# Optimization experiments

Measured on AMD Instinct MI355X. Metric: run time of the kernel, lower is better.

Reference implementation:

```python
import jax, jax.numpy as jnp
import numpy as np

EPS = 1e-09
TOP_K = 2


def setup_inputs() -> dict:
    key = jax.random.key(0)
    ks = jax.random.split(key, 6)
    B, L, F, E, D, SE = 64, 1024, 900, 8, 768, 64
    cycle_curve_data = jax.random.normal(ks[0], (B, L, F), dtype=jnp.float32)
    logits = jax.random.normal(ks[1], (B, E), dtype=jnp.float32)
    moe_masks = jax.random.randint(ks[2], (B, E), 0, 2, dtype=jnp.int32)
    selection_embeddings = jax.random.normal(ks[3], (B, E, SE), dtype=jnp.float32)
    W = jax.random.normal(ks[4], (E, F, D), dtype=jnp.float32) * 0.02
    b = jnp.zeros((E, D), dtype=jnp.float32)
    return {"cycle_curve_data": cycle_curve_data, "logits": logits,
            "moe_masks": moe_masks, "selection_embeddings": selection_embeddings,
            "W": W, "b": b}


def reference(cycle_curve_data, logits, moe_masks, selection_embeddings, W, b):
    B = cycle_curve_data.shape[0]
    E = logits.shape[1]
    mask = (moe_masks == 1).astype(logits.dtype)                 # [B, E]
    raw = jax.nn.softmax(logits, axis=1)                         # [B, E]
    p = raw * mask
    # selection embedding from inactive experts
    inactive = raw * (1.0 - mask)
    inactive = inactive / (jnp.sum(inactive, axis=1, keepdims=True) + EPS)
    selection_embedding = jnp.sum(selection_embeddings * inactive[:, :, None], axis=1)  # [B, SE]
    # top-k masking (indices treated as constants, same as torch scatter mask)
    if TOP_K > 0:
        _, idx = jax.lax.top_k(p, TOP_K)                         # [B, K]
        topk_mask = jnp.zeros_like(p).at[jnp.arange(B)[:, None], idx].set(1.0)
        p = p * topk_mask
    p = p / (jnp.sum(p, axis=1, keepdims=True) + EPS)            # [B, E]
    # dispatch/combine == weighted sum of per-expert Linear outputs
    # (weights are zero for unselected experts, matching MOEDispatcher)
    out = jnp.zeros(cycle_curve_data.shape[:2] + (W.shape[-1],), dtype=cycle_curve_data.dtype)
    for e in range(E):  # small fixed expert count
        expert_out = jnp.einsum('blf,fd->bld', cycle_curve_data, W[e]) + b[e]
        out = out + p[:, e, None, None] * expert_out
    final_out = out.astype(jnp.bfloat16)
    # guide loss (training mode)
    s = jnp.sum(raw * mask) / B
    guide_loss = (1.0 - s) * (1.0 - s)
    return final_out, guide_loss, selection_embedding
```

## Files before the change

kernel.cpp:

```cpp
#include <hip/hip_runtime.h>

#define B_  64
#define L_  1024
#define F_  900
#define E_  8
#define D_  768
#define SE_ 64
#define KP_ 928
#define FD_ (F_*D_)
#define OUT_MAIN (64*1024*768)
#define GL_OFF   OUT_MAIN
#define SE_OFF   (OUT_MAIN + 1)
#define EPSF 1e-9f


using f32x4  = __attribute__((ext_vector_type(4))) float;
using bf16   = __bf16;
using bf16x4 = __attribute__((ext_vector_type(4))) __bf16;
using bf16x8 = __attribute__((ext_vector_type(8))) __bf16;
using s16x8  = __attribute__((ext_vector_type(8))) short;

__device__ __forceinline__ f32x4 mfma_bf16(bf16x8 a, bf16x8 b, f32x4 c) {
  return __builtin_amdgcn_mfma_f32_16x16x32_bf16(
      __builtin_bit_cast(s16x8, a), __builtin_bit_cast(s16x8, b), c, 0, 0, 0);
}

__device__ __forceinline__ const unsigned* pick_masks(const void* cA, const void* cB,
                                                      const float** logits) {
  const unsigned* a = (const unsigned*)cA;
  bool aIsMask = true;
#pragma unroll
  for (int i = 0; i < 512; i += 37) aIsMask &= (a[i] <= 1u);
  if (aIsMask) { *logits = (const float*)cB; return a; }
  *logits = (const float*)cA; return (const unsigned*)cB;
}

struct Gate { int e1, e2; float p1, p2; };

__device__ __forceinline__ Gate gate_for(const float* __restrict__ logits,
                                         const unsigned* __restrict__ masks, int b) {
  float lg[E_]; unsigned mk[E_];
#pragma unroll
  for (int e = 0; e < E_; ++e) { lg[e] = logits[b*E_+e]; mk[e] = masks[b*E_+e]; }
  float mx = lg[0];
#pragma unroll
  for (int e = 1; e < E_; ++e) mx = fmaxf(mx, lg[e]);
  float ex[E_], s = 0.f;
#pragma unroll
  for (int e = 0; e < E_; ++e) { ex[e] = expf(lg[e]-mx); s += ex[e]; }
  const float inv_s = 1.f / s;
  float p0[E_];
#pragma unroll
  for (int e = 0; e < E_; ++e) p0[e] = (mk[e] == 1u) ? ex[e]*inv_s : 0.f;
  int e1 = 0;
#pragma unroll
  for (int e = 1; e < E_; ++e) if (p0[e] > p0[e1]) e1 = e;
  int e2 = (e1 == 0) ? 1 : 0;
#pragma unroll
  for (int e = 0; e < E_; ++e) if (e != e1 && p0[e] > p0[e2]) e2 = e;
  const float inv = 1.f / (p0[e1] + p0[e2] + EPSF);
  Gate g; g.e1 = e1; g.e2 = e2; g.p1 = p0[e1]*inv; g.p2 = p0[e2]*inv;
  return g;
}

__global__ void gating_kernel(const void* cA, const void* cB,
                              const float* __restrict__ selemb,
                              float* __restrict__ fout) {
  const float* logits; const unsigned* masks = pick_masks(cA, cB, &logits);
  const int b = threadIdx.x;
  float lg[E_]; unsigned mk[E_];
#pragma unroll
  for (int e = 0; e < E_; ++e) { lg[e] = logits[b*E_+e]; mk[e] = masks[b*E_+e]; }
  float mx = lg[0];
#pragma unroll
  for (int e = 1; e < E_; ++e) mx = fmaxf(mx, lg[e]);
  float ex[E_], s = 0.f;
#pragma unroll
  for (int e = 0; e < E_; ++e) { ex[e] = expf(lg[e]-mx); s += ex[e]; }
  const float inv_s = 1.f / s;
  float inact[E_]; float isum = 0.f, sact = 0.f;
#pragma unroll
  for (int e = 0; e < E_; ++e) {
    float raw = ex[e] * inv_s;
    if (mk[e] == 1u) { sact += raw; inact[e] = 0.f; }
    else             { inact[e] = raw; isum += raw; }
  }
  const float inv_i = 1.f / (isum + EPSF);
  for (int se = 0; se < SE_; ++se) {
    float a = 0.f;
#pragma unroll
    for (int e = 0; e < E_; ++e)
      a += inact[e] * inv_i * selemb[((size_t)b*E_ + e)*SE_ + se];
    fout[SE_OFF + b*SE_ + se] = a;
  }
#pragma unroll
  for (int off = 32; off > 0; off >>= 1) sact += __shfl_down(sact, off);
  if (b == 0) {
    float sm = sact / (float)B_;
    fout[GL_OFF] = (1.f - sm) * (1.f - sm);
  }
}

__global__ void transw_kernel(const float* __restrict__ W,
                              bf16* __restrict__ Wt) {
  __shared__ float tile[32][33];
  const int e  = blockIdx.z;
  const int d0 = blockIdx.x << 5;
  const int f0 = blockIdx.y << 5;
  const int c = threadIdx.x & 31, r = threadIdx.x >> 5;
#pragma unroll
  for (int p = 0; p < 4; ++p) {
    int f = f0 + p*8 + r;
    tile[p*8+r][c] = (f < F_) ? W[((size_t)e*F_ + f)*D_ + d0 + c] : 0.f;
  }
  __syncthreads();
#pragma unroll
  for (int p = 0; p < 4; ++p) {
    int d = d0 + p*8 + r;
    Wt[((size_t)e*D_ + d)*KP_ + f0 + c] = (bf16)tile[c][p*8+r];
  }
}

__global__ __launch_bounds__(256) void gemm_kernel(
    const float* __restrict__ X, const bf16* __restrict__ Wt,
    const float* __restrict__ bias,
    const void* cA, const void* cB,
    float* __restrict__ fout) {
  __shared__ bf16 As[128][40];
  __shared__ bf16 Bs[128][40];

  const int bn = blockIdx.x, bm = blockIdx.y, b = blockIdx.z;
  const float* logits; const unsigned* masks = pick_masks(cA, cB, &logits);
  const Gate g = gate_for(logits, masks, b);
  const int e1 = g.e1, e2 = g.e2;
  const float p1 = g.p1, p2 = g.p2;

  const float* Xb = X + ((size_t)b*L_ + (size_t)bm*128) * F_;
  const bf16* W1 = Wt + ((size_t)e1*D_ + (size_t)bn*128) * KP_;
  const bf16* W2 = Wt + ((size_t)e2*D_ + (size_t)bn*128) * KP_;

  const int t  = threadIdx.x;
  const int ar = t >> 3, ac = (t & 7) << 2;
  const int br = t >> 2, bc = (t & 3) << 3;

  const int lane = t & 63, wave = t >> 6;
  const int wr = (wave >> 1) << 6, wc = (wave & 1) << 6;
  const int fr = lane & 15, fk = (lane >> 4) << 3;
  const int rq = (lane >> 4) << 2;

  f32x4 acc[4][4];
#pragma unroll
  for (int m = 0; m < 4; ++m)
#pragma unroll
    for (int n = 0; n < 4; ++n) acc[m][n] = (f32x4){0.f,0.f,0.f,0.f};

  f32x4  ax[4];
  bf16x8 wv1[2], wv2[2];

  auto LOAD = [&](int k0) {
    if (k0 <= F_ - 32) {
#pragma unroll
      for (int p = 0; p < 4; ++p)
        ax[p] = *(const f32x4*)(Xb + (size_t)(p*32 + ar)*F_ + k0 + ac);
    } else {
#pragma unroll
      for (int p = 0; p < 4; ++p)
#pragma unroll
        for (int j = 0; j < 4; ++j) {
          int k = k0 + ac + j;
          ax[p][j] = (k < F_) ? Xb[(size_t)(p*32 + ar)*F_ + k] : 0.f;
        }
    }
#pragma unroll
    for (int p = 0; p < 2; ++p) {
      wv1[p] = *(const bf16x8*)(W1 + (size_t)(p*64 + br)*KP_ + k0 + bc);
      wv2[p] = *(const bf16x8*)(W2 + (size_t)(p*64 + br)*KP_ + k0 + bc);
    }
  };

  auto STAGE = [&]() {
#pragma unroll
    for (int p = 0; p < 4; ++p) {
      bf16x4 v;
#pragma unroll
      for (int j = 0; j < 4; ++j) v[j] = (bf16)ax[p][j];
      *(bf16x4*)&As[p*32 + ar][ac] = v;
    }
#pragma unroll
    for (int p = 0; p < 2; ++p) {
      bf16x8 v;
#pragma unroll
      for (int j = 0; j < 8; ++j)
        v[j] = (bf16)(p1 * (float)wv1[p][j] + p2 * (float)wv2[p][j]);
      *(bf16x8*)&Bs[p*64 + br][bc] = v;
    }
  };

  LOAD(0);
  const int NT = 29;
  for (int kt = 0; kt < NT; ++kt) {
    STAGE();
    __syncthreads();
    if (kt + 1 < NT) LOAD((kt + 1) << 5);
    bf16x8 af[4], bfv[4];
#pragma unroll
    for (int m = 0; m < 4; ++m) af[m]  = *(const bf16x8*)&As[wr + m*16 + fr][fk];
#pragma unroll
    for (int n = 0; n < 4; ++n) bfv[n] = *(const bf16x8*)&Bs[wc + n*16 + fr][fk];
#pragma unroll
    for (int m = 0; m < 4; ++m)
#pragma unroll
      for (int n = 0; n < 4; ++n)
        acc[m][n] = mfma_bf16(af[m], bfv[n], acc[m][n]);
    __syncthreads();
  }

  const float* b1 = bias + e1*D_;
  const float* b2 = bias + e2*D_;
#pragma unroll
  for (int n = 0; n < 4; ++n) {
    int gc = bn*128 + wc + n*16 + fr;
    float bs = p1*b1[gc] + p2*b2[gc];
#pragma unroll
    for (int m = 0; m < 4; ++m) {
      size_t base = ((size_t)b*L_ + (size_t)(bm*128 + wr + m*16 + rq)) * D_ + gc;
#pragma unroll
      for (int i = 0; i < 4; ++i)
        fout[base + (size_t)i*D_] = acc[m][n][i] + bs;
    }
  }
}

__global__ __launch_bounds__(128) void fallback_kernel(
    const float* __restrict__ X, const float* __restrict__ W,
    const float* __restrict__ bias,
    const void* cA, const void* cB,
    float* __restrict__ fout) {
  __shared__ float xs[16 * F_];
  const int t  = threadIdx.x;
  const int d  = blockIdx.x * 128 + t;
  const int l0 = blockIdx.y * 16;
  const int b  = blockIdx.z;
  const float* logits; const unsigned* masks = pick_masks(cA, cB, &logits);
  const Gate g = gate_for(logits, masks, b);

  const float* xrow = X + ((size_t)b*L_ + l0) * F_;
  for (int i = t; i < 16 * F_; i += 128) xs[i] = xrow[i];
  __syncthreads();

  const float* w1 = W + (size_t)g.e1*FD_ + d;
  const float* w2 = W + (size_t)g.e2*FD_ + d;
  float acc[16];
#pragma unroll
  for (int j = 0; j < 16; ++j) acc[j] = 0.f;

  for (int k = 0; k < F_; k += 4) {
    float wb[4];
#pragma unroll
    for (int q = 0; q < 4; ++q)
      wb[q] = g.p1 * w1[(size_t)(k+q)*D_] + g.p2 * w2[(size_t)(k+q)*D_];
#pragma unroll
    for (int j = 0; j < 16; ++j) {
      f32x4 xv = *(const f32x4*)&xs[j*F_ + k];
#pragma unroll
      for (int q = 0; q < 4; ++q) acc[j] += xv[q] * wb[q];
    }
  }

  const float bs = g.p1*bias[g.e1*D_+d] + g.p2*bias[g.e2*D_+d];
#pragma unroll
  for (int j = 0; j < 16; ++j)
    fout[((size_t)b*L_ + (size_t)(l0 + j)) * D_ + d] = acc[j] + bs;
}

extern "C" void kernel_launch(void* const* d_in, const int* in_sizes, int n_in,
                              void* d_out, int out_size, void* d_ws, size_t ws_size,
                              hipStream_t stream) {
  const float *X = nullptr, *selemb = nullptr, *W = nullptr, *bias = nullptr;
  const void *cA = nullptr, *cB = nullptr;
  for (int i = 0; i < n_in; ++i) {
    switch (in_sizes[i]) {
      case 58982400: X      = (const float*)d_in[i]; break;
      case 32768:    selemb = (const float*)d_in[i]; break;
      case 5529600:  W      = (const float*)d_in[i]; break;
      case 6144:     bias   = (const float*)d_in[i]; break;
      case 512:      if (!cA) cA = d_in[i]; else cB = d_in[i]; break;
      default: break;
    }
  }
  if (!X)      X      = (const float*)d_in[0];
  if (!cA)     cA     = d_in[1];
  if (!cB)     cB     = d_in[2];
  if (!selemb) selemb = (const float*)d_in[3];
  if (!W)      W      = (const float*)d_in[4];
  if (!bias)   bias   = (const float*)d_in[5];
  float* fout = (float*)d_out;

  bf16* Wt = (bf16*)d_ws;
  const bool full = (ws_size >= (size_t)E_*D_*KP_*2);

  gating_kernel<<<1, 64, 0, stream>>>(cA, cB, selemb, fout);
  if (full) {
    transw_kernel<<<dim3(24, 29, 8), 256, 0, stream>>>(W, Wt);
    gemm_kernel<<<dim3(6, 8, 64), 256, 0, stream>>>(X, Wt, bias, cA, cB, fout);
  } else {
    fallback_kernel<<<dim3(6, 64, 64), 128, 0, stream>>>(X, W, bias, cA, cB, fout);
  }
}
```

Before: 370.2 us.

## Pre-convert X to bf16, premix per-batch weights, use direct-to-LDS double-buffered GEMM

```diff
diff --git a/kernel.cpp b/kernel.cpp
--- a/kernel.cpp
+++ b/kernel.cpp
@@ -12,6 +12,7 @@
 #define GL_OFF   OUT_MAIN
 #define SE_OFF   (OUT_MAIN + 1)
 #define EPSF 1e-9f
+#define NT_  29
 
 
 using f32x4  = __attribute__((ext_vector_type(4))) float;
@@ -23,6 +24,12 @@
 __device__ __forceinline__ f32x4 mfma_bf16(bf16x8 a, bf16x8 b, f32x4 c) {
   return __builtin_amdgcn_mfma_f32_16x16x32_bf16(
       __builtin_bit_cast(s16x8, a), __builtin_bit_cast(s16x8, b), c, 0, 0, 0);
+}
+
+__device__ __forceinline__ void gload16(const bf16* g, bf16* l) {
+  __builtin_amdgcn_global_load_lds(
+      (const __attribute__((address_space(1))) unsigned int*)g,
+      (__attribute__((address_space(3))) unsigned int*)l, 16, 0, 0);
 }
 
 __device__ __forceinline__ const unsigned* pick_masks(const void* cA, const void* cB,
@@ -101,8 +108,143 @@
   }
 }
 
-__global__ void transw_kernel(const float* __restrict__ W,
-                              bf16* __restrict__ Wt) {
+__global__ __launch_bounds__(256) void xconv_kernel(const float* __restrict__ X,
+                                                    bf16* __restrict__ Xbf) {
+  const size_t row = blockIdx.x;
+  const int t = threadIdx.x;
+  const float* src = X + row * F_;
+  bf16* dst = Xbf + row * KP_;
+  if (t < 225) {
+    f32x4 v = *(const f32x4*)(src + t*4);
+    bf16x4 o;
+#pragma unroll
+    for (int j = 0; j < 4; ++j) o[j] = (bf16)v[j];
+    *(bf16x4*)(dst + t*4) = o;
+  } else if (t < 232) {
+    bf16x4 z = (bf16x4){(bf16)0.f,(bf16)0.f,(bf16)0.f,(bf16)0.f};
+    *(bf16x4*)(dst + 900 + (t-225)*4) = z;
+  }
+}
+
+__global__ __launch_bounds__(256) void wmix_kernel(const float* __restrict__ W,
+                                                   const void* cA, const void* cB,
+                                                   bf16* __restrict__ Wmix) {
+  __shared__ float tile[32][33];
+  const int b  = blockIdx.z;
+  const int d0 = blockIdx.x << 5;
+  const int f0 = blockIdx.y << 5;
+  const float* logits; const unsigned* masks = pick_masks(cA, cB, &logits);
+  const Gate g = gate_for(logits, masks, b);
+  const float* W1 = W + (size_t)g.e1*FD_;
+  const float* W2 = W + (size_t)g.e2*FD_;
+  const int c = threadIdx.x & 31, r = threadIdx.x >> 5;
+#pragma unroll
+  for (int p = 0; p < 4; ++p) {
+    int f = f0 + p*8 + r;
+    float v = 0.f;
+    if (f < F_) {
+      size_t o = (size_t)f*D_ + d0 + c;
+      v = g.p1*W1[o] + g.p2*W2[o];
+    }
+    tile[p*8+r][c] = v;
+  }
+  __syncthreads();
+#pragma unroll
+  for (int p = 0; p < 4; ++p) {
+    int d = d0 + p*8 + r;
+    Wmix[((size_t)b*D_ + d)*KP_ + f0 + c] = (bf16)tile[c][p*8+r];
+  }
+}
+
+__global__ __launch_bounds__(256) void gemm_fast(
+    const bf16* __restrict__ Xbf, const bf16* __restrict__ Wmix,
+    const float* __restrict__ bias,
+    const void* cA, const void* cB,
+    float* __restrict__ fout) {
+  __shared__ bf16 As[2][128*32];
+  __shared__ bf16 Bs[2][128*32];
+
+  const int id  = blockIdx.x;
+  const int xcd = id & 7, q = id >> 3;
+  const int b   = xcd + ((q / 48) << 3);
+  const int j   = q % 48;
+  const int bn  = j % 6, bm = j / 6;
+
+  const float* logits; const unsigned* masks = pick_masks(cA, cB, &logits);
+  const Gate g = gate_for(logits, masks, b);
+
+  const bf16* Ab = Xbf  + ((size_t)b*L_ + (size_t)bm*128) * KP_;
+  const bf16* Bb = Wmix + ((size_t)b*D_ + (size_t)bn*128) * KP_;
+
+  const int t = threadIdx.x, lane = t & 63, w = t >> 6;
+  const int sw   = ((lane & 3) ^ ((lane >> 2) & 3)) << 3;
+  const int row0 = (w << 5) + (lane >> 2);
+  const int row1 = row0 + 16;
+  const int dst0 = (w << 7) << 3;
+  const int dst1 = dst0 + (64 << 3);
+
+  auto STAGE = [&](int buf, int kt) {
+    const int k0 = kt << 5;
+    gload16(Ab + (size_t)row0*KP_ + k0 + sw, &As[buf][dst0]);
+    gload16(Ab + (size_t)row1*KP_ + k0 + sw, &As[buf][dst1]);
+    gload16(Bb + (size_t)row0*KP_ + k0 + sw, &Bs[buf][dst0]);
+    gload16(Bb + (size_t)row1*KP_ + k0 + sw, &Bs[buf][dst1]);
+  };
+
+  const int wr = (w >> 1) << 6, wc = (w & 1) << 6;
+  const int fr = lane & 15, fks = lane >> 4;
+  const int rq = (lane >> 4) << 2;
+
+  int aoff[4], boff[4];
+#pragma unroll
+  for (int m = 0; m < 4; ++m) {
+    int rA = wr + m*16 + fr;
+    aoff[m] = rA*32 + ((fks ^ (rA & 3)) << 3);
+    int rB = wc + m*16 + fr;
+    boff[m] = rB*32 + ((fks ^ (rB & 3)) << 3);
+  }
+
+  f32x4 acc[4][4];
+#pragma unroll
+  for (int m = 0; m < 4; ++m)
+#pragma unroll
+    for (int n = 0; n < 4; ++n) acc[m][n] = (f32x4){0.f,0.f,0.f,0.f};
+
+  STAGE(0, 0);
+  int cur = 0;
+  for (int kt = 0; kt < NT_; ++kt) {
+    __syncthreads();
+    if (kt + 1 < NT_) STAGE(cur ^ 1, kt + 1);
+    bf16x8 af[4], bfv[4];
+#pragma unroll
+    for (int m = 0; m < 4; ++m) af[m]  = *(const bf16x8*)&As[cur][aoff[m]];
+#pragma unroll
+    for (int n = 0; n < 4; ++n) bfv[n] = *(const bf16x8*)&Bs[cur][boff[n]];
+#pragma unroll
+    for (int m = 0; m < 4; ++m)
+#pragma unroll
+      for (int n = 0; n < 4; ++n)
+        acc[m][n] = mfma_bf16(af[m], bfv[n], acc[m][n]);
+    cur ^= 1;
+  }
+
+  const float* b1 = bias + g.e1*D_;
+  const float* b2 = bias + g.e2*D_;
+#pragma unroll
+  for (int n = 0; n < 4; ++n) {
+    int gc = bn*128 + wc + n*16 + fr;
+    float bs = g.p1*b1[gc] + g.p2*b2[gc];
+#pragma unroll
+    for (int m = 0; m < 4; ++m) {
+      size_t base = ((size_t)b*L_ + (size_t)(bm*128 + wr + m*16 + rq)) * D_ + gc;
+#pragma unroll
+      for (int i = 0; i < 4; ++i)
+        fout[base + (size_t)i*D_] = acc[m][n][i] + bs;
+    }
+  }
+}
+
+__global__ void transw_kernel(const float* __restrict__ W, bf16* __restrict__ Wt) {
   __shared__ float tile[32][33];
   const int e  = blockIdx.z;
   const int d0 = blockIdx.x << 5;
@@ -128,35 +270,25 @@
     float* __restrict__ fout) {
   __shared__ bf16 As[128][40];
   __shared__ bf16 Bs[128][40];
-
   const int bn = blockIdx.x, bm = blockIdx.y, b = blockIdx.z;
   const float* logits; const unsigned* masks = pick_masks(cA, cB, &logits);
   const Gate g = gate_for(logits, masks, b);
-  const int e1 = g.e1, e2 = g.e2;
-  const float p1 = g.p1, p2 = g.p2;
-
   const float* Xb = X + ((size_t)b*L_ + (size_t)bm*128) * F_;
-  const bf16* W1 = Wt + ((size_t)e1*D_ + (size_t)bn*128) * KP_;
-  const bf16* W2 = Wt + ((size_t)e2*D_ + (size_t)bn*128) * KP_;
-
+  const bf16* W1 = Wt + ((size_t)g.e1*D_ + (size_t)bn*128) * KP_;
+  const bf16* W2 = Wt + ((size_t)g.e2*D_ + (size_t)bn*128) * KP_;
   const int t  = threadIdx.x;
   const int ar = t >> 3, ac = (t & 7) << 2;
   const int br = t >> 2, bc = (t & 3) << 3;
-
   const int lane = t & 63, wave = t >> 6;
   const int wr = (wave >> 1) << 6, wc = (wave & 1) << 6;
   const int fr = lane & 15, fk = (lane >> 4) << 3;
   const int rq = (lane >> 4) << 2;
-
   f32x4 acc[4][4];
 #pragma unroll
   for (int m = 0; m < 4; ++m)
 #pragma unroll
     for (int n = 0; n < 4; ++n) acc[m][n] = (f32x4){0.f,0.f,0.f,0.f};
-
-  f32x4  ax[4];
-  bf16x8 wv1[2], wv2[2];
-
+  f32x4 ax[4]; bf16x8 wv1[2], wv2[2];
   auto LOAD = [&](int k0) {
     if (k0 <= F_ - 32) {
 #pragma unroll
@@ -177,7 +309,6 @@
       wv2[p] = *(const bf16x8*)(W2 + (size_t)(p*64 + br)*KP_ + k0 + bc);
     }
   };
-
   auto STAGE = [&]() {
 #pragma unroll
     for (int p = 0; p < 4; ++p) {
@@ -191,17 +322,15 @@
       bf16x8 v;
 #pragma unroll
       for (int j = 0; j < 8; ++j)
-        v[j] = (bf16)(p1 * (float)wv1[p][j] + p2 * (float)wv2[p][j]);
+        v[j] = (bf16)(g.p1 * (float)wv1[p][j] + g.p2 * (float)wv2[p][j]);
       *(bf16x8*)&Bs[p*64 + br][bc] = v;
     }
   };
-
   LOAD(0);
-  const int NT = 29;
-  for (int kt = 0; kt < NT; ++kt) {
+  for (int kt = 0; kt < NT_; ++kt) {
     STAGE();
     __syncthreads();
-    if (kt + 1 < NT) LOAD((kt + 1) << 5);
+    if (kt + 1 < NT_) LOAD((kt + 1) << 5);
     bf16x8 af[4], bfv[4];
 #pragma unroll
     for (int m = 0; m < 4; ++m) af[m]  = *(const bf16x8*)&As[wr + m*16 + fr][fk];
@@ -214,13 +343,12 @@
         acc[m][n] = mfma_bf16(af[m], bfv[n], acc[m][n]);
     __syncthreads();
   }
-
-  const float* b1 = bias + e1*D_;
-  const float* b2 = bias + e2*D_;
+  const float* b1 = bias + g.e1*D_;
+  const float* b2 = bias + g.e2*D_;
 #pragma unroll
   for (int n = 0; n < 4; ++n) {
     int gc = bn*128 + wc + n*16 + fr;
-    float bs = p1*b1[gc] + p2*b2[gc];
+    float bs = g.p1*b1[gc] + g.p2*b2[gc];
 #pragma unroll
     for (int m = 0; m < 4; ++m) {
       size_t base = ((size_t)b*L_ + (size_t)(bm*128 + wr + m*16 + rq)) * D_ + gc;
@@ -243,17 +371,14 @@
   const int b  = blockIdx.z;
   const float* logits; const unsigned* masks = pick_masks(cA, cB, &logits);
   const Gate g = gate_for(logits, masks, b);
-
   const float* xrow = X + ((size_t)b*L_ + l0) * F_;
   for (int i = t; i < 16 * F_; i += 128) xs[i] = xrow[i];
   __syncthreads();
-
   const float* w1 = W + (size_t)g.e1*FD_ + d;
   const float* w2 = W + (size_t)g.e2*FD_ + d;
   float acc[16];
 #pragma unroll
   for (int j = 0; j < 16; ++j) acc[j] = 0.f;
-
   for (int k = 0; k < F_; k += 4) {
     float wb[4];
 #pragma unroll
@@ -266,7 +391,6 @@
       for (int q = 0; q < 4; ++q) acc[j] += xv[q] * wb[q];
     }
   }
-
   const float bs = g.p1*bias[g.e1*D_+d] + g.p2*bias[g.e2*D_+d];
 #pragma unroll
   for (int j = 0; j < 16; ++j)
@@ -296,11 +420,21 @@
   if (!bias)   bias   = (const float*)d_in[5];
   float* fout = (float*)d_out;
 
-  bf16* Wt = (bf16*)d_ws;
-  const bool full = (ws_size >= (size_t)E_*D_*KP_*2);
+  const size_t xbf_bytes  = (size_t)B_*L_*KP_*2;
+  const size_t wmix_bytes = (size_t)B_*D_*KP_*2;
+  const size_t need_fast  = xbf_bytes + wmix_bytes;
+  const size_t need_mid   = (size_t)E_*D_*KP_*2;
 
   gating_kernel<<<1, 64, 0, stream>>>(cA, cB, selemb, fout);
-  if (full) {
+
+  if (ws_size >= need_fast) {
+    bf16* Xbf  = (bf16*)d_ws;
+    bf16* Wmix = (bf16*)((char*)d_ws + xbf_bytes);
+    xconv_kernel<<<B_*L_, 256, 0, stream>>>(X, Xbf);
+    wmix_kernel<<<dim3(24, 29, 64), 256, 0, stream>>>(W, cA, cB, Wmix);
+    gemm_fast<<<3072, 256, 0, stream>>>(Xbf, Wmix, bias, cA, cB, fout);
+  } else if (ws_size >= need_mid) {
+    bf16* Wt = (bf16*)d_ws;
     transw_kernel<<<dim3(24, 29, 8), 256, 0, stream>>>(W, Wt);
     gemm_kernel<<<dim3(6, 8, 64), 256, 0, stream>>>(X, Wt, bias, cA, cB, fout);
   } else {
```

Result: slower. 417.6 us (+12.8%).

## Double-buffer GEMM with direct global-to-LDS loads, swizzled LDS and XCD-aware block mapping

Applied to the files above, without the earlier changes.

```diff
diff --git a/kernel.cpp b/kernel.cpp
--- a/kernel.cpp
+++ b/kernel.cpp
@@ -12,6 +12,7 @@
 #define GL_OFF   OUT_MAIN
 #define SE_OFF   (OUT_MAIN + 1)
 #define EPSF 1e-9f
+#define NT_  29
 
 
 using f32x4  = __attribute__((ext_vector_type(4))) float;
@@ -23,6 +24,12 @@
 __device__ __forceinline__ f32x4 mfma_bf16(bf16x8 a, bf16x8 b, f32x4 c) {
   return __builtin_amdgcn_mfma_f32_16x16x32_bf16(
       __builtin_bit_cast(s16x8, a), __builtin_bit_cast(s16x8, b), c, 0, 0, 0);
+}
+
+__device__ __forceinline__ void gload16(const bf16* g, bf16* l) {
+  __builtin_amdgcn_global_load_lds(
+      (const __attribute__((address_space(1))) unsigned int*)g,
+      (__attribute__((address_space(3))) unsigned int*)l, 16, 0, 0);
 }
 
 __device__ __forceinline__ const unsigned* pick_masks(const void* cA, const void* cB,
@@ -101,8 +108,7 @@
   }
 }
 
-__global__ void transw_kernel(const float* __restrict__ W,
-                              bf16* __restrict__ Wt) {
+__global__ void transw_kernel(const float* __restrict__ W, bf16* __restrict__ Wt) {
   __shared__ float tile[32][33];
   const int e  = blockIdx.z;
   const int d0 = blockIdx.x << 5;
@@ -121,112 +127,146 @@
   }
 }
 
-__global__ __launch_bounds__(256) void gemm_kernel(
+__global__ __launch_bounds__(256) void gemm_fast(
     const float* __restrict__ X, const bf16* __restrict__ Wt,
     const float* __restrict__ bias,
     const void* cA, const void* cB,
     float* __restrict__ fout) {
-  __shared__ bf16 As[128][40];
-  __shared__ bf16 Bs[128][40];
-
-  const int bn = blockIdx.x, bm = blockIdx.y, b = blockIdx.z;
+  __shared__ bf16 As [2][128*32];
+  __shared__ bf16 B1s[2][128*32];
+  __shared__ bf16 B2s[2][128*32];
+
+  const int id  = blockIdx.x;
+  const int xcd = id & 7, q = id >> 3;
+  const int b   = xcd + ((q / 48) << 3);
+  const int j   = q % 48;
+  const int bn  = j % 6, bm = j / 6;
+
   const float* logits; const unsigned* masks = pick_masks(cA, cB, &logits);
   const Gate g = gate_for(logits, masks, b);
-  const int e1 = g.e1, e2 = g.e2;
-  const float p1 = g.p1, p2 = g.p2;
-
-  const float* Xb = X + ((size_t)b*L_ + (size_t)bm*128) * F_;
-  const bf16* W1 = Wt + ((size_t)e1*D_ + (size_t)bn*128) * KP_;
-  const bf16* W2 = Wt + ((size_t)e2*D_ + (size_t)bn*128) * KP_;
-
-  const int t  = threadIdx.x;
-  const int ar = t >> 3, ac = (t & 7) << 2;
-  const int br = t >> 2, bc = (t & 3) << 3;
-
-  const int lane = t & 63, wave = t >> 6;
-  const int wr = (wave >> 1) << 6, wc = (wave & 1) << 6;
-  const int fr = lane & 15, fk = (lane >> 4) << 3;
+
+  const float* Xb = X  + ((size_t)b*L_ + (size_t)bm*128) * F_;
+  const bf16*  W1 = Wt + ((size_t)g.e1*D_ + (size_t)bn*128) * KP_;
+  const bf16*  W2 = Wt + ((size_t)g.e2*D_ + (size_t)bn*128) * KP_;
+
+  const int t = threadIdx.x, lane = t & 63, w = t >> 6;
+
+  const int sw   = ((lane & 3) ^ ((lane >> 2) & 3)) << 3;
+  const int row0 = (w << 5) + (lane >> 2);
+  const int row1 = row0 + 16;
+  const int dst0 = (w << 7) << 3;
+  const int dst1 = dst0 + (64 << 3);
+
+  auto STAGE_B = [&](int buf, int kt) {
+    const int k0 = kt << 5;
+    gload16(W1 + (size_t)row0*KP_ + k0 + sw, &B1s[buf][dst0]);
+    gload16(W1 + (size_t)row1*KP_ + k0 + sw, &B1s[buf][dst1]);
+    gload16(W2 + (size_t)row0*KP_ + k0 + sw, &B2s[buf][dst0]);
+    gload16(W2 + (size_t)row1*KP_ + k0 + sw, &B2s[buf][dst1]);
+  };
+
+  const int arow = t >> 1, akh = t & 1;
+  const float* Asrc = Xb + (size_t)arow*F_ + akh*16;
+  const int aw0 = arow*32 + ((((akh<<1)|0) ^ (arow & 3)) << 3);
+  const int aw1 = arow*32 + ((((akh<<1)|1) ^ (arow & 3)) << 3);
+
+  f32x4 ax[4];
+  auto LOAD_A = [&](int kt) {
+    const int k0 = kt << 5;
+    if (kt < NT_ - 1) {
+#pragma unroll
+      for (int i = 0; i < 4; ++i) ax[i] = *(const f32x4*)(Asrc + k0 + i*4);
+    } else {
+#pragma unroll
+      for (int i = 0; i < 4; ++i)
+#pragma unroll
+        for (int jj = 0; jj < 4; ++jj) {
+          int k = k0 + akh*16 + i*4 + jj;
+          ax[i][jj] = (k < F_) ? Xb[(size_t)arow*F_ + k] : 0.f;
+        }
+    }
+  };
+  auto WRITE_A = [&](int buf) {
+    bf16x8 v0, v1;
+#pragma unroll
+    for (int jj = 0; jj < 4; ++jj) {
+      v0[jj] = (bf16)ax[0][jj]; v0[4+jj] = (bf16)ax[1][jj];
+      v1[jj] = (bf16)ax[2][jj]; v1[4+jj] = (bf16)ax[3][jj];
+    }
+    *(bf16x8*)&As[buf][aw0] = v0;
+    *(bf16x8*)&As[buf][aw1] = v1;
+  };
+
+  const int wr = (w >> 1) << 6, wc = (w & 1) << 6;
+  const int fr = lane & 15, fks = lane >> 4;
   const int rq = (lane >> 4) << 2;
 
-  f32x4 acc[4][4];
+  int aoff[4], boff[4];
+#pragma unroll
+  for (int m = 0; m < 4; ++m) {
+    int rA = wr + m*16 + fr;
+    aoff[m] = rA*32 + ((fks ^ (rA & 3)) << 3);
+    int rB = wc + m*16 + fr;
+    boff[m] = rB*32 + ((fks ^ (rB & 3)) << 3);
+  }
+
+  f32x4 acc1[4][4], acc2[4][4];
 #pragma unroll
   for (int m = 0; m < 4; ++m)
 #pragma unroll
-    for (int n = 0; n < 4; ++n) acc[m][n] = (f32x4){0.f,0.f,0.f,0.f};
-
-  f32x4  ax[4];
-  bf16x8 wv1[2], wv2[2];
-
-  auto LOAD = [&](int k0) {
-    if (k0 <= F_ - 32) {
-#pragma unroll
-      for (int p = 0; p < 4; ++p)
-        ax[p] = *(const f32x4*)(Xb + (size_t)(p*32 + ar)*F_ + k0 + ac);
+    for (int n = 0; n < 4; ++n) {
+      acc1[m][n] = (f32x4){0.f,0.f,0.f,0.f};
+      acc2[m][n] = (f32x4){0.f,0.f,0.f,0.f};
+    }
+
+  LOAD_A(0);
+  STAGE_B(0, 0);
+  int cur = 0;
+#pragma unroll 1
+  for (int kt = 0; kt < NT_; ++kt) {
+    WRITE_A(cur);
+    if (kt + 1 < NT_) {
+      LOAD_A(kt + 1);
+      STAGE_B(cur ^ 1, kt + 1);
+      asm volatile("s_waitcnt vmcnt(8)" ::: "memory");
     } else {
-#pragma unroll
-      for (int p = 0; p < 4; ++p)
-#pragma unroll
-        for (int j = 0; j < 4; ++j) {
-          int k = k0 + ac + j;
-          ax[p][j] = (k < F_) ? Xb[(size_t)(p*32 + ar)*F_ + k] : 0.f;
-        }
-    }
-#pragma unroll
-    for (int p = 0; p < 2; ++p) {
-      wv1[p] = *(const bf16x8*)(W1 + (size_t)(p*64 + br)*KP_ + k0 + bc);
-      wv2[p] = *(const bf16x8*)(W2 + (size_t)(p*64 + br)*KP_ + k0 + bc);
-    }
-  };
-
-  auto STAGE = [&]() {
-#pragma unroll
-    for (int p = 0; p < 4; ++p) {
-      bf16x4 v;
-#pragma unroll
-      for (int j = 0; j < 4; ++j) v[j] = (bf16)ax[p][j];
-      *(bf16x4*)&As[p*32 + ar][ac] = v;
-    }
-#pragma unroll
-    for (int p = 0; p < 2; ++p) {
-      bf16x8 v;
-#pragma unroll
-      for (int j = 0; j < 8; ++j)
-        v[j] = (bf16)(p1 * (float)wv1[p][j] + p2 * (float)wv2[p][j]);
-      *(bf16x8*)&Bs[p*64 + br][bc] = v;
-    }
-  };
-
-  LOAD(0);
-  const int NT = 29;
-  for (int kt = 0; kt < NT; ++kt) {
-    STAGE();
-    __syncthreads();
-    if (kt + 1 < NT) LOAD((kt + 1) << 5);
-    bf16x8 af[4], bfv[4];
-#pragma unroll
-    for (int m = 0; m < 4; ++m) af[m]  = *(const bf16x8*)&As[wr + m*16 + fr][fk];
-#pragma unroll
-    for (int n = 0; n < 4; ++n) bfv[n] = *(const bf16x8*)&Bs[wc + n*16 + fr][fk];
+      asm volatile("s_waitcnt vmcnt(0)" ::: "memory");
+    }
+    asm volatile("s_waitcnt lgkmcnt(0)" ::: "memory");
+    __builtin_amdgcn_sched_barrier(0);
+    __builtin_amdgcn_s_barrier();
+    __builtin_amdgcn_sched_barrier(0);
+    bf16x8 af[4], b1f[4], b2f[4];
+#pragma unroll
+    for (int m = 0; m < 4; ++m) af[m]  = *(const bf16x8*)&As [cur][aoff[m]];
+#pragma unroll
+    for (int n = 0; n < 4; ++n) b1f[n] = *(const bf16x8*)&B1s[cur][boff[n]];
+#pragma unroll
+    for (int n = 0; n < 4; ++n) b2f[n] = *(const bf16x8*)&B2s[cur][boff[n]];
 #pragma unroll
     for (int m = 0; m < 4; ++m)
 #pragma unroll
-      for (int n = 0; n < 4; ++n)
-        acc[m][n] = mfma_bf16(af[m], bfv[n], acc[m][n]);
-    __syncthreads();
-  }
-
-  const float* b1 = bias + e1*D_;
-  const float* b2 = bias + e2*D_;
+      for (int n = 0; n < 4; ++n) {
+        acc1[m][n] = mfma_bf16(af[m], b1f[n], acc1[m][n]);
+        acc2[m][n] = mfma_bf16(af[m], b2f[n], acc2[m][n]);
+      }
+    __builtin_amdgcn_sched_barrier(0);
+    __builtin_amdgcn_s_barrier();
+    cur ^= 1;
+  }
+
+  const float* b1 = bias + g.e1*D_;
+  const float* b2 = bias + g.e2*D_;
 #pragma unroll
   for (int n = 0; n < 4; ++n) {
     int gc = bn*128 + wc + n*16 + fr;
-    float bs = p1*b1[gc] + p2*b2[gc];
+    float bs = g.p1*b1[gc] + g.p2*b2[gc];
 #pragma unroll
     for (int m = 0; m < 4; ++m) {
       size_t base = ((size_t)b*L_ + (size_t)(bm*128 + wr + m*16 + rq)) * D_ + gc;
 #pragma unroll
       for (int i = 0; i < 4; ++i)
-        fout[base + (size_t)i*D_] = acc[m][n][i] + bs;
+        fout[base + (size_t)i*D_] = g.p1*acc1[m][n][i] + g.p2*acc2[m][n][i] + bs;
     }
   }
 }
@@ -243,17 +283,14 @@
   const int b  = blockIdx.z;
   const float* logits; const unsigned* masks = pick_masks(cA, cB, &logits);
   const Gate g = gate_for(logits, masks, b);
-
   const float* xrow = X + ((size_t)b*L_ + l0) * F_;
   for (int i = t; i < 16 * F_; i += 128) xs[i] = xrow[i];
   __syncthreads();
-
   const float* w1 = W + (size_t)g.e1*FD_ + d;
   const float* w2 = W + (size_t)g.e2*FD_ + d;
   float acc[16];
 #pragma unroll
   for (int j = 0; j < 16; ++j) acc[j] = 0.f;
-
   for (int k = 0; k < F_; k += 4) {
     float wb[4];
 #pragma unroll
@@ -266,7 +303,6 @@
       for (int q = 0; q < 4; ++q) acc[j] += xv[q] * wb[q];
     }
   }
-
   const float bs = g.p1*bias[g.e1*D_+d] + g.p2*bias[g.e2*D_+d];
 #pragma unroll
   for (int j = 0; j < 16; ++j)
@@ -296,13 +332,13 @@
   if (!bias)   bias   = (const float*)d_in[5];
   float* fout = (float*)d_out;
 
-  bf16* Wt = (bf16*)d_ws;
-  const bool full = (ws_size >= (size_t)E_*D_*KP_*2);
+  const size_t need = (size_t)E_*D_*KP_*2;
 
   gating_kernel<<<1, 64, 0, stream>>>(cA, cB, selemb, fout);
-  if (full) {
+  if (ws_size >= need) {
+    bf16* Wt = (bf16*)d_ws;
     transw_kernel<<<dim3(24, 29, 8), 256, 0, stream>>>(W, Wt);
-    gemm_kernel<<<dim3(6, 8, 64), 256, 0, stream>>>(X, Wt, bias, cA, cB, fout);
+    gemm_fast<<<3072, 256, 0, stream>>>(X, Wt, bias, cA, cB, fout);
   } else {
     fallback_kernel<<<dim3(6, 64, 64), 128, 0, stream>>>(X, W, bias, cA, cB, fout);
   }
```

Result: slower. 543.5 us (+46.8%).
